# Kernel optimization log

Measured on AMD Instinct MI355X. Metric: run time of the kernel, lower is better.

Reference implementation:

```python
import jax, jax.numpy as jnp
import numpy as np

LPOS, LDIR, H = 10, 4, 256
N = 262144


def posenc(x, L):
    freqs = (2.0 ** jnp.arange(L)).astype(x.dtype)  # [L]
    ang = x[:, None, :] * freqs[:, None]            # [N, L, 3]
    sc = jnp.concatenate([jnp.sin(ang), jnp.cos(ang)], axis=-1)  # [N, L, 6]
    return jnp.concatenate([x, sc.reshape(x.shape[0], L * 6)], axis=1)


def _lin(key, fan_in, fan_out):
    k1, k2 = jax.random.split(key)
    bound = 1.0 / np.sqrt(fan_in)
    w = jax.random.uniform(k1, (fan_out, fan_in), jnp.float32, -bound, bound)
    b = jax.random.uniform(k2, (fan_out,), jnp.float32, -bound, bound)
    return w, b


def setup_inputs() -> dict:
    key = jax.random.key(0)
    ks = jax.random.split(key, 16)
    inp = {
        'xyz': jax.random.normal(ks[0], (N, 3), jnp.float32),
        'd': jax.random.normal(ks[1], (N, 3), jnp.float32),
    }
    in1 = LPOS * 6 + 3  # 63
    dims1 = [(in1, H), (H, H), (H, H), (H, H), (H, H)]
    for i, (fi, fo) in enumerate(dims1):
        w, b = _lin(ks[2 + i], fi, fo)
        inp[f'w1_{i}'], inp[f'b1_{i}'] = w, b
    dims2 = [(H + in1, H), (H, H), (H, H), (H, H + 1)]
    for i, (fi, fo) in enumerate(dims2):
        w, b = _lin(ks[7 + i], fi, fo)
        inp[f'w2_{i}'], inp[f'b2_{i}'] = w, b
    w, b = _lin(ks[11], H + LDIR * 6 + 3, H // 2)
    inp['wr0'], inp['br0'] = w, b
    w, b = _lin(ks[12], H // 2, 3)
    inp['wr1'], inp['br1'] = w, b
    return inp


def reference(xyz, d,
              w1_0, b1_0, w1_1, b1_1, w1_2, b1_2, w1_3, b1_3, w1_4, b1_4,
              w2_0, b2_0, w2_1, b2_1, w2_2, b2_2, w2_3, b2_3,
              wr0, br0, wr1, br1):
    relu = jax.nn.relu
    x_emb = posenc(xyz, LPOS)  # [N, 63]
    d_emb = posenc(d, LDIR)    # [N, 27]
    h = x_emb
    for w, b in ((w1_0, b1_0), (w1_1, b1_1), (w1_2, b1_2), (w1_3, b1_3), (w1_4, b1_4)):
        h = relu(h @ w.T + b)
    h = jnp.concatenate([h, x_emb], axis=1)
    for w, b in ((w2_0, b2_0), (w2_1, b2_1), (w2_2, b2_2)):
        h = relu(h @ w.T + b)
    h = h @ w2_3.T + b2_3  # [N, H+1]
    sigma = h[:, -1]
    h = h[:, :-1]
    # rgb head
    g = relu(jnp.concatenate([h, d_emb], axis=1) @ wr0.T + br0)
    c = jax.nn.sigmoid(g @ wr1.T + br1)  # [N, 3]
    return c, relu(sigma)
```

## Files before the change

kernel.cpp:

```cpp
#include <hip/hip_runtime.h>
#include <hip/hip_bf16.h>

#define NPTS 262144
#define ROWS 64
#define FR 512
#define BUF1_OFF 16384
#define XBUF_OFF 32768
#define LDS_BYTES ((16384*2 + 4096)*2)

typedef __attribute__((ext_vector_type(8))) short short8;
typedef __attribute__((ext_vector_type(4))) float f32x4;

__device__ __forceinline__ ushort bfu(float f) {
  union { float f; unsigned u; } x; x.f = f;
  unsigned r = x.u + 0x7fffu + ((x.u >> 16) & 1u);
  return (ushort)(r >> 16);
}
__device__ __forceinline__ unsigned pk2(float a, float b) {
  __hip_bfloat162 h = __float22bfloat162_rn(float2{a, b});
  return *reinterpret_cast<unsigned*>(&h);
}

__global__ void pack_w(const float* __restrict__ w, ushort* __restrict__ dst,
                       int OUT, int KIN, int nct, int nkt) {
  int t = blockIdx.x * 256 + threadIdx.x;
  int total = nct * nkt * 64;
  if (t >= total) return;
  int l  = t & 63;
  int kt = (t >> 6) % nkt;
  int ct = (t >> 6) / nkt;
  int row = ct * 16 + (l & 15);
  int k0  = kt * 32 + (l >> 4) * 8;
  ushort* d = dst + (size_t)t * 8;
  #pragma unroll
  for (int j = 0; j < 8; ++j) {
    int k = k0 + j;
    float v = (row < OUT && k < KIN) ? w[(size_t)row * KIN + k] : 0.f;
    d[j] = bfu(v);
  }
}

__global__ void pack_b(const float* __restrict__ b, float* __restrict__ dst, int OUT, int OUTP) {
  int i = blockIdx.x * 256 + threadIdx.x;
  if (i < OUTP) dst[i] = (i < OUT) ? b[i] : 0.f;
}

template<int NKT, int KSPLIT, int NC, bool RELU>
__device__ __forceinline__ void layerg(
    const ushort* __restrict__ wpk, const float* __restrict__ bias,
    const ushort* a0, const ushort* a1, int rs1,
    ushort* dst, int ctBase, int lane)
{
  const int lr = lane & 15, lk = lane >> 4;
  f32x4 acc[4][NC];
  #pragma unroll
  for (int c = 0; c < NC; ++c) {
    f32x4 b4 = *(const f32x4*)(bias + (ctBase + c) * 16 + lk * 4);
    #pragma unroll
    for (int r = 0; r < 4; ++r) acc[r][c] = b4;
  }
  #pragma unroll
  for (int kt = 0; kt < NKT; ++kt) {
    short8 av[4];
    #pragma unroll
    for (int r = 0; r < 4; ++r) {
      const ushort* src = (kt < KSPLIT)
        ? (a0 + (r * 8 + kt) * FR + lane * 8)
        : (a1 + (r * rs1 + (kt - KSPLIT)) * FR + lane * 8);
      av[r] = *(const short8*)src;
    }
    #pragma unroll
    for (int c = 0; c < NC; ++c) {
      short8 bv = *(const short8*)(wpk + (size_t)(((ctBase + c) * NKT + kt) * 64 + lane) * 8);
      #pragma unroll
      for (int r = 0; r < 4; ++r)
        acc[r][c] = __builtin_amdgcn_mfma_f32_16x16x32_bf16(bv, av[r], acc[r][c], 0, 0, 0);
    }
  }
  #pragma unroll
  for (int c = 0; c < NC; ++c) {
    const int ct = ctBase + c;
    const int Lp = lr + 16 * ((ct & 1) * 2 + (lk >> 1));
    const int kq = ct >> 1;
    #pragma unroll
    for (int r = 0; r < 4; ++r) {
      float v0 = acc[r][c][0], v1 = acc[r][c][1], v2 = acc[r][c][2], v3 = acc[r][c][3];
      if (RELU) {
        v0 = fmaxf(v0, 0.f); v1 = fmaxf(v1, 0.f);
        v2 = fmaxf(v2, 0.f); v3 = fmaxf(v3, 0.f);
      }
      uint2 p; p.x = pk2(v0, v1); p.y = pk2(v2, v3);
      *(uint2*)(dst + (r * 8 + kq) * FR + Lp * 8 + (lk & 1) * 4) = p;
    }
  }
}

extern __shared__ ushort smem[];

__global__ __launch_bounds__(512, 4) void nerf_fused(
    const float* __restrict__ xyz, const float* __restrict__ dvec,
    const ushort* __restrict__ wp, const float* __restrict__ bp,
    float* __restrict__ out)
{
  ushort* buf0 = smem;
  ushort* buf1 = smem + BUF1_OFF;
  ushort* xbuf = smem + XBUF_OFF;
  const int tid  = threadIdx.x;
  const int row0 = blockIdx.x * ROWS;
  const int wave = tid >> 6, lane = tid & 63;
  const int lr = lane & 15, lk = lane >> 4;

  {
    const int r = wave & 3, kt = wave >> 2;
    const float* x = xyz + (size_t)(row0 + r * 16 + lr) * 3;
    float xv[3] = {x[0], x[1], x[2]};
    const int c0 = kt * 32 + lk * 8;
    unsigned u[4];
    #pragma unroll
    for (int q = 0; q < 4; ++q) {
      ushort h2[2];
      #pragma unroll
      for (int hh = 0; hh < 2; ++hh) {
        int c = c0 + q * 2 + hh;
        float v;
        if (c < 3) v = xv[c];
        else if (c < 63) {
          int idx = c - 3, l = idx / 6, t = idx - l * 6;
          float f = (float)(1 << l);
          float xx = xv[t < 3 ? t : t - 3];
          v = (t < 3) ? __sinf(xx * f) : __cosf(xx * f);
        } else v = 0.f;
        h2[hh] = bfu(v);
      }
      u[q] = (unsigned)h2[0] | ((unsigned)h2[1] << 16);
    }
    uint4* dstv = (uint4*)(xbuf + (r * 2 + kt) * FR + lane * 8);
    *dstv = make_uint4(u[0], u[1], u[2], u[3]);
  }
  __syncthreads();
  layerg<2, 0, 2, true >(wp + 0,      bp + 0,    buf0, xbuf, 2, buf0, wave * 2, lane);
  __syncthreads();
  layerg<8, 8, 2, true >(wp + 16384,  bp + 256,  buf0, xbuf, 2, buf1, wave * 2, lane);
  __syncthreads();
  layerg<8, 8, 2, true >(wp + 81920,  bp + 512,  buf1, xbuf, 2, buf0, wave * 2, lane);
  __syncthreads();
  layerg<8, 8, 2, true >(wp + 147456, bp + 768,  buf0, xbuf, 2, buf1, wave * 2, lane);
  __syncthreads();
  layerg<8, 8, 2, true >(wp + 212992, bp + 1024, buf1, xbuf, 2, buf0, wave * 2, lane);
  __syncthreads();
  layerg<10, 8, 2, true>(wp + 278528, bp + 1280, buf0, xbuf, 2, buf1, wave * 2, lane);
  __syncthreads();
  if (wave < 4) {
    const int r = wave;
    const float* d = dvec + (size_t)(row0 + r * 16 + lr) * 3;
    float dv[3] = {d[0], d[1], d[2]};
    const int c0 = lk * 8;
    unsigned u[4];
    #pragma unroll
    for (int q = 0; q < 4; ++q) {
      ushort h2[2];
      #pragma unroll
      for (int hh = 0; hh < 2; ++hh) {
        int c = c0 + q * 2 + hh;
        float v;
        if (c < 3) v = dv[c];
        else if (c < 27) {
          int idx = c - 3, l = idx / 6, t = idx - l * 6;
          float f = (float)(1 << l);
          float xx = dv[t < 3 ? t : t - 3];
          v = (t < 3) ? __sinf(xx * f) : __cosf(xx * f);
        } else v = 0.f;
        h2[hh] = bfu(v);
      }
      u[q] = (unsigned)h2[0] | ((unsigned)h2[1] << 16);
    }
    uint4* dstv = (uint4*)(xbuf + r * FR + lane * 8);
    *dstv = make_uint4(u[0], u[1], u[2], u[3]);
  }
  layerg<8, 8, 2, true >(wp + 360448, bp + 1536, buf1, xbuf, 2, buf0, wave * 2, lane);
  __syncthreads();
  layerg<8, 8, 2, true >(wp + 425984, bp + 1792, buf0, xbuf, 2, buf1, wave * 2, lane);
  __syncthreads();
  layerg<8, 8, 2, false>(wp + 491520, bp + 2048, buf1, xbuf, 2, buf0, wave * 2, lane);
  if (wave == 0) {
    const ushort* w23 = wp + 491520;
    float bb = bp[2048 + 256 + lr];
    f32x4 acc2[4];
    #pragma unroll
    for (int r = 0; r < 4; ++r) acc2[r] = (f32x4){bb, bb, bb, bb};
    #pragma unroll
    for (int kt = 0; kt < 8; ++kt) {
      short8 bv = *(const short8*)(w23 + (size_t)((16 * 8 + kt) * 64 + lane) * 8);
      #pragma unroll
      for (int r = 0; r < 4; ++r) {
        short8 av = *(const short8*)(buf1 + (r * 8 + kt) * FR + lane * 8);
        acc2[r] = __builtin_amdgcn_mfma_f32_16x16x32_bf16(av, bv, acc2[r], 0, 0, 0);
      }
    }
    if (lr == 0) {
      #pragma unroll
      for (int r = 0; r < 4; ++r)
        #pragma unroll
        for (int i = 0; i < 4; ++i)
          out[(size_t)3 * NPTS + row0 + r * 16 + lk * 4 + i] = fmaxf(acc2[r][i], 0.f);
    }
  }
  __syncthreads();
  layerg<9, 8, 1, true>(wp + 561152, bp + 2320, buf0, xbuf, 1, buf1, wave, lane);
  __syncthreads();
  if (wave < 4) {
    const ushort* w = wp + 598016;
    float bb = bp[2448 + lr];
    f32x4 acc = (f32x4){bb, bb, bb, bb};
    #pragma unroll
    for (int kt = 0; kt < 4; ++kt) {
      short8 av = *(const short8*)(buf1 + (wave * 8 + kt) * FR + lane * 8);
      short8 bv = *(const short8*)(w + (size_t)(kt * 64 + lane) * 8);
      acc = __builtin_amdgcn_mfma_f32_16x16x32_bf16(av, bv, acc, 0, 0, 0);
    }
    if (lr < 3) {
      #pragma unroll
      for (int i = 0; i < 4; ++i) {
        int grow = row0 + wave * 16 + lk * 4 + i;
        out[(size_t)grow * 3 + lr] = 1.f / (1.f + __expf(-acc[i]));
      }
    }
  }
}

extern "C" void kernel_launch(void* const* d_in, const int* in_sizes, int n_in,
                              void* d_out, int out_size, void* d_ws, size_t ws_size,
                              hipStream_t stream) {
  const float* xyz  = (const float*)d_in[0];
  const float* dvec = (const float*)d_in[1];
  ushort* wp = (ushort*)d_ws;
  float*  bp = (float*)((char*)d_ws + 1200128);

  struct WSpec { int idx, OUT, KIN, nct, nkt, off; };
  const WSpec wspecs[11] = {
    { 2, 256,  63, 16,  2,      0},
    { 4, 256, 256, 16,  8,  16384},
    { 6, 256, 256, 16,  8,  81920},
    { 8, 256, 256, 16,  8, 147456},
    {10, 256, 256, 16,  8, 212992},
    {12, 256, 319, 16, 10, 278528},
    {14, 256, 256, 16,  8, 360448},
    {16, 256, 256, 16,  8, 425984},
    {18, 257, 256, 17,  8, 491520},
    {20, 128, 283,  8,  9, 561152},
    {22,   3, 128,  1,  4, 598016},
  };
  for (int i = 0; i < 11; ++i) {
    int total = wspecs[i].nct * wspecs[i].nkt * 64;
    pack_w<<<dim3((total + 255) / 256), dim3(256), 0, stream>>>(
      (const float*)d_in[wspecs[i].idx], wp + wspecs[i].off,
      wspecs[i].OUT, wspecs[i].KIN, wspecs[i].nct, wspecs[i].nkt);
  }
  struct BSpec { int idx, OUT, OUTP, off; };
  const BSpec bspecs[11] = {
    { 3, 256, 256,    0}, { 5, 256, 256,  256}, { 7, 256, 256,  512}, { 9, 256, 256,  768},
    {11, 256, 256, 1024}, {13, 256, 256, 1280}, {15, 256, 256, 1536}, {17, 256, 256, 1792},
    {19, 257, 272, 2048}, {21, 128, 128, 2320}, {23,   3,  16, 2448},
  };
  for (int i = 0; i < 11; ++i) {
    pack_b<<<dim3((bspecs[i].OUTP + 255) / 256), dim3(256), 0, stream>>>(
      (const float*)d_in[bspecs[i].idx], bp + bspecs[i].off, bspecs[i].OUT, bspecs[i].OUTP);
  }

  hipFuncSetAttribute(reinterpret_cast<const void*>(nerf_fused),
                      hipFuncAttributeMaxDynamicSharedMemorySize, LDS_BYTES);
  nerf_fused<<<dim3(NPTS / ROWS), dim3(512), LDS_BYTES, stream>>>(xyz, dvec, wp, bp, (float*)d_out);
}
```

Baseline: 338.1 us.

## Switch fused NeRF MLP from 16x16x32 to 32x32x16 bf16 MFMA tiles

Replaces the 16x16x32 MFMA instruction with 32x32x16 across all layers. The packed weight layout, LDS activation layout, positional-encoding writers, bias padding and workspace offsets all change to match 32-row, 16-k fragments. Each wave now owns one 32-column output tile over two 32-row groups instead of two 16-column tiles over four row groups. The larger tiles give more MACs per operand load and fewer LDS and global weight fetches per FLOP. In exchange each wave holds larger accumulators, which raises register pressure.

```diff
diff --git a/kernel.cpp b/kernel.cpp
--- a/kernel.cpp
+++ b/kernel.cpp
@@ -3,13 +3,13 @@
 
 #define NPTS 262144
 #define ROWS 64
-#define FR 512
 #define BUF1_OFF 16384
 #define XBUF_OFF 32768
 #define LDS_BYTES ((16384*2 + 4096)*2)
 
-typedef __attribute__((ext_vector_type(8))) short short8;
-typedef __attribute__((ext_vector_type(4))) float f32x4;
+typedef __attribute__((ext_vector_type(8)))  short short8;
+typedef __attribute__((ext_vector_type(4)))  float f32x4;
+typedef __attribute__((ext_vector_type(16))) float f32x16;
 
 __device__ __forceinline__ ushort bfu(float f) {
   union { float f; unsigned u; } x; x.f = f;
@@ -29,8 +29,8 @@
   int l  = t & 63;
   int kt = (t >> 6) % nkt;
   int ct = (t >> 6) / nkt;
-  int row = ct * 16 + (l & 15);
-  int k0  = kt * 32 + (l >> 4) * 8;
+  int row = ct * 32 + (l & 31);
+  int k0  = kt * 16 + (l >> 5) * 8;
   ushort* d = dst + (size_t)t * 8;
   #pragma unroll
   for (int j = 0; j < 8; ++j) {
@@ -45,54 +45,67 @@
   if (i < OUTP) dst[i] = (i < OUT) ? b[i] : 0.f;
 }
 
-template<int NKT, int KSPLIT, int NC, bool RELU>
+template<int NKT, int KSPLIT, int NR, bool RELU>
 __device__ __forceinline__ void layerg(
     const ushort* __restrict__ wpk, const float* __restrict__ bias,
-    const ushort* a0, const ushort* a1, int rs1,
-    ushort* dst, int ctBase, int lane)
+    const ushort* a0, int s0, const ushort* a1, int s1,
+    ushort* dst, int ct, int r2base, int lane)
 {
-  const int lr = lane & 15, lk = lane >> 4;
-  f32x4 acc[4][NC];
-  #pragma unroll
-  for (int c = 0; c < NC; ++c) {
-    f32x4 b4 = *(const f32x4*)(bias + (ctBase + c) * 16 + lk * 4);
-    #pragma unroll
-    for (int r = 0; r < 4; ++r) acc[r][c] = b4;
-  }
+  const int l5 = lane >> 5;
+  f32x4 bq[4];
+  #pragma unroll
+  for (int qq = 0; qq < 4; ++qq)
+    bq[qq] = *(const f32x4*)(bias + ct * 32 + qq * 8 + 4 * l5);
+  f32x16 acc[NR];
+  #pragma unroll
+  for (int rr = 0; rr < NR; ++rr)
+    #pragma unroll
+    for (int qq = 0; qq < 4; ++qq) {
+      acc[rr][qq * 4 + 0] = bq[qq][0];
+      acc[rr][qq * 4 + 1] = bq[qq][1];
+      acc[rr][qq * 4 + 2] = bq[qq][2];
+      acc[rr][qq * 4 + 3] = bq[qq][3];
+    }
   #pragma unroll
   for (int kt = 0; kt < NKT; ++kt) {
-    short8 av[4];
-    #pragma unroll
-    for (int r = 0; r < 4; ++r) {
+    short8 bv = *(const short8*)(wpk + (size_t)((ct * NKT + kt) * 64 + lane) * 8);
+    #pragma unroll
+    for (int rr = 0; rr < NR; ++rr) {
+      const int r2 = r2base + rr;
       const ushort* src = (kt < KSPLIT)
-        ? (a0 + (r * 8 + kt) * FR + lane * 8)
-        : (a1 + (r * rs1 + (kt - KSPLIT)) * FR + lane * 8);
-      av[r] = *(const short8*)src;
-    }
-    #pragma unroll
-    for (int c = 0; c < NC; ++c) {
-      short8 bv = *(const short8*)(wpk + (size_t)(((ctBase + c) * NKT + kt) * 64 + lane) * 8);
-      #pragma unroll
-      for (int r = 0; r < 4; ++r)
-        acc[r][c] = __builtin_amdgcn_mfma_f32_16x16x32_bf16(bv, av[r], acc[r][c], 0, 0, 0);
-    }
-  }
-  #pragma unroll
-  for (int c = 0; c < NC; ++c) {
-    const int ct = ctBase + c;
-    const int Lp = lr + 16 * ((ct & 1) * 2 + (lk >> 1));
-    const int kq = ct >> 1;
-    #pragma unroll
-    for (int r = 0; r < 4; ++r) {
-      float v0 = acc[r][c][0], v1 = acc[r][c][1], v2 = acc[r][c][2], v3 = acc[r][c][3];
+          ? a0 + (r2 * s0 + kt) * 512 + lane * 8
+          : a1 + (r2 * s1 + (kt - KSPLIT)) * 512 + lane * 8;
+      short8 av = *(const short8*)src;
+      acc[rr] = __builtin_amdgcn_mfma_f32_32x32x16_bf16(bv, av, acc[rr], 0, 0, 0);
+    }
+  }
+  #pragma unroll
+  for (int rr = 0; rr < NR; ++rr) {
+    const int r2 = r2base + rr;
+    #pragma unroll
+    for (int qq = 0; qq < 4; ++qq) {
+      float v0 = acc[rr][qq * 4 + 0], v1 = acc[rr][qq * 4 + 1];
+      float v2 = acc[rr][qq * 4 + 2], v3 = acc[rr][qq * 4 + 3];
       if (RELU) {
         v0 = fmaxf(v0, 0.f); v1 = fmaxf(v1, 0.f);
         v2 = fmaxf(v2, 0.f); v3 = fmaxf(v3, 0.f);
       }
       uint2 p; p.x = pk2(v0, v1); p.y = pk2(v2, v3);
-      *(uint2*)(dst + (r * 8 + kq) * FR + Lp * 8 + (lk & 1) * 4) = p;
-    }
-  }
+      *(uint2*)(dst + (r2 * 16 + ct * 2 + (qq >> 1)) * 512
+                    + ((lane & 31) + 32 * (qq & 1)) * 8 + 4 * l5) = p;
+    }
+  }
+}
+
+__device__ __forceinline__ float pe_val(const float xv[3], int c, int CMAX) {
+  if (c < 3) return xv[c];
+  if (c < CMAX) {
+    int idx = c - 3, l = idx / 6, t = idx - l * 6;
+    float f = (float)(1 << l);
+    float xx = xv[t < 3 ? t : t - 3];
+    return (t < 3) ? __sinf(xx * f) : __cosf(xx * f);
+  }
+  return 0.f;
 }
 
 extern __shared__ ushort smem[];
@@ -108,122 +121,93 @@
   const int tid  = threadIdx.x;
   const int row0 = blockIdx.x * ROWS;
   const int wave = tid >> 6, lane = tid & 63;
-  const int lr = lane & 15, lk = lane >> 4;
+  const int l5 = lane >> 5;
 
   {
-    const int r = wave & 3, kt = wave >> 2;
-    const float* x = xyz + (size_t)(row0 + r * 16 + lr) * 3;
+    const int r2 = wave >> 2, kt = wave & 3;
+    const float* x = xyz + (size_t)(row0 + r2 * 32 + (lane & 31)) * 3;
     float xv[3] = {x[0], x[1], x[2]};
-    const int c0 = kt * 32 + lk * 8;
+    const int c0 = kt * 16 + l5 * 8;
     unsigned u[4];
     #pragma unroll
-    for (int q = 0; q < 4; ++q) {
-      ushort h2[2];
-      #pragma unroll
-      for (int hh = 0; hh < 2; ++hh) {
-        int c = c0 + q * 2 + hh;
-        float v;
-        if (c < 3) v = xv[c];
-        else if (c < 63) {
-          int idx = c - 3, l = idx / 6, t = idx - l * 6;
-          float f = (float)(1 << l);
-          float xx = xv[t < 3 ? t : t - 3];
-          v = (t < 3) ? __sinf(xx * f) : __cosf(xx * f);
-        } else v = 0.f;
-        h2[hh] = bfu(v);
-      }
-      u[q] = (unsigned)h2[0] | ((unsigned)h2[1] << 16);
-    }
-    uint4* dstv = (uint4*)(xbuf + (r * 2 + kt) * FR + lane * 8);
-    *dstv = make_uint4(u[0], u[1], u[2], u[3]);
-  }
-  __syncthreads();
-  layerg<2, 0, 2, true >(wp + 0,      bp + 0,    buf0, xbuf, 2, buf0, wave * 2, lane);
-  __syncthreads();
-  layerg<8, 8, 2, true >(wp + 16384,  bp + 256,  buf0, xbuf, 2, buf1, wave * 2, lane);
-  __syncthreads();
-  layerg<8, 8, 2, true >(wp + 81920,  bp + 512,  buf1, xbuf, 2, buf0, wave * 2, lane);
-  __syncthreads();
-  layerg<8, 8, 2, true >(wp + 147456, bp + 768,  buf0, xbuf, 2, buf1, wave * 2, lane);
-  __syncthreads();
-  layerg<8, 8, 2, true >(wp + 212992, bp + 1024, buf1, xbuf, 2, buf0, wave * 2, lane);
-  __syncthreads();
-  layerg<10, 8, 2, true>(wp + 278528, bp + 1280, buf0, xbuf, 2, buf1, wave * 2, lane);
+    for (int q = 0; q < 4; ++q)
+      u[q] = (unsigned)bfu(pe_val(xv, c0 + q * 2, 63))
+           | ((unsigned)bfu(pe_val(xv, c0 + q * 2 + 1, 63)) << 16);
+    *(uint4*)(xbuf + (r2 * 4 + kt) * 512 + lane * 8) = make_uint4(u[0], u[1], u[2], u[3]);
+  }
+  __syncthreads();
+  layerg<4, 0, 2, true >(wp + 0,      bp + 0,    xbuf, 4, xbuf, 4, buf0, wave, 0, lane);
+  __syncthreads();
+  layerg<16, 16, 2, true>(wp + 16384,  bp + 256,  buf0, 16, buf0, 16, buf1, wave, 0, lane);
+  __syncthreads();
+  layerg<16, 16, 2, true>(wp + 81920,  bp + 512,  buf1, 16, buf1, 16, buf0, wave, 0, lane);
+  __syncthreads();
+  layerg<16, 16, 2, true>(wp + 147456, bp + 768,  buf0, 16, buf0, 16, buf1, wave, 0, lane);
+  __syncthreads();
+  layerg<16, 16, 2, true>(wp + 212992, bp + 1024, buf1, 16, buf1, 16, buf0, wave, 0, lane);
+  __syncthreads();
+  layerg<20, 16, 2, true>(wp + 278528, bp + 1280, buf0, 16, xbuf, 4, buf1, wave, 0, lane);
   __syncthreads();
   if (wave < 4) {
-    const int r = wave;
-    const float* d = dvec + (size_t)(row0 + r * 16 + lr) * 3;
+    const int r2 = wave >> 1, kt = wave & 1;
+    const float* d = dvec + (size_t)(row0 + r2 * 32 + (lane & 31)) * 3;
     float dv[3] = {d[0], d[1], d[2]};
-    const int c0 = lk * 8;
+    const int c0 = kt * 16 + l5 * 8;
     unsigned u[4];
     #pragma unroll
-    for (int q = 0; q < 4; ++q) {
-      ushort h2[2];
-      #pragma unroll
-      for (int hh = 0; hh < 2; ++hh) {
-        int c = c0 + q * 2 + hh;
-        float v;
-        if (c < 3) v = dv[c];
-        else if (c < 27) {
-          int idx = c - 3, l = idx / 6, t = idx - l * 6;
-          float f = (float)(1 << l);
-          float xx = dv[t < 3 ? t : t - 3];
-          v = (t < 3) ? __sinf(xx * f) : __cosf(xx * f);
-        } else v = 0.f;
-        h2[hh] = bfu(v);
-      }
-      u[q] = (unsigned)h2[0] | ((unsigned)h2[1] << 16);
-    }
-    uint4* dstv = (uint4*)(xbuf + r * FR + lane * 8);
-    *dstv = make_uint4(u[0], u[1], u[2], u[3]);
-  }
-  layerg<8, 8, 2, true >(wp + 360448, bp + 1536, buf1, xbuf, 2, buf0, wave * 2, lane);
-  __syncthreads();
-  layerg<8, 8, 2, true >(wp + 425984, bp + 1792, buf0, xbuf, 2, buf1, wave * 2, lane);
-  __syncthreads();
-  layerg<8, 8, 2, false>(wp + 491520, bp + 2048, buf1, xbuf, 2, buf0, wave * 2, lane);
-  if (wave == 0) {
+    for (int q = 0; q < 4; ++q)
+      u[q] = (unsigned)bfu(pe_val(dv, c0 + q * 2, 27))
+           | ((unsigned)bfu(pe_val(dv, c0 + q * 2 + 1, 27)) << 16);
+    *(uint4*)(xbuf + (r2 * 2 + kt) * 512 + lane * 8) = make_uint4(u[0], u[1], u[2], u[3]);
+  }
+  layerg<16, 16, 2, true>(wp + 360448, bp + 1536, buf1, 16, buf1, 16, buf0, wave, 0, lane);
+  __syncthreads();
+  layerg<16, 16, 2, true>(wp + 425984, bp + 1792, buf0, 16, buf0, 16, buf1, wave, 0, lane);
+  __syncthreads();
+  layerg<16, 16, 2, false>(wp + 491520, bp + 2048, buf1, 16, buf1, 16, buf0, wave, 0, lane);
+  if (wave < 2) {
     const ushort* w23 = wp + 491520;
-    float bb = bp[2048 + 256 + lr];
-    f32x4 acc2[4];
-    #pragma unroll
-    for (int r = 0; r < 4; ++r) acc2[r] = (f32x4){bb, bb, bb, bb};
+    const int r2 = wave;
+    f32x16 acc;
+    #pragma unroll
+    for (int qq = 0; qq < 4; ++qq) {
+      f32x4 b4 = *(const f32x4*)(bp + 2048 + 256 + qq * 8 + 4 * l5);
+      acc[qq * 4 + 0] = b4[0]; acc[qq * 4 + 1] = b4[1];
+      acc[qq * 4 + 2] = b4[2]; acc[qq * 4 + 3] = b4[3];
+    }
+    #pragma unroll
+    for (int kt = 0; kt < 16; ++kt) {
+      short8 bv = *(const short8*)(w23 + (size_t)((8 * 16 + kt) * 64 + lane) * 8);
+      short8 av = *(const short8*)(buf1 + (r2 * 16 + kt) * 512 + lane * 8);
+      acc = __builtin_amdgcn_mfma_f32_32x32x16_bf16(bv, av, acc, 0, 0, 0);
+    }
+    if (lane < 32)
+      out[(size_t)3 * NPTS + row0 + r2 * 32 + lane] = fmaxf(acc[0], 0.f);
+  }
+  __syncthreads();
+  layerg<18, 16, 1, true>(wp + 565248, bp + 2336, buf0, 16, xbuf, 2, buf1, wave & 3, wave >> 2, lane);
+  __syncthreads();
+  if (wave < 2) {
+    const ushort* w = wp + 602112;
+    const int r2 = wave;
+    f32x16 acc;
+    #pragma unroll
+    for (int qq = 0; qq < 4; ++qq) {
+      f32x4 b4 = *(const f32x4*)(bp + 2464 + qq * 8 + 4 * l5);
+      acc[qq * 4 + 0] = b4[0]; acc[qq * 4 + 1] = b4[1];
+      acc[qq * 4 + 2] = b4[2]; acc[qq * 4 + 3] = b4[3];
+    }
     #pragma unroll
     for (int kt = 0; kt < 8; ++kt) {
-      short8 bv = *(const short8*)(w23 + (size_t)((16 * 8 + kt) * 64 + lane) * 8);
-      #pragma unroll
-      for (int r = 0; r < 4; ++r) {
-        short8 av = *(const short8*)(buf1 + (r * 8 + kt) * FR + lane * 8);
-        acc2[r] = __builtin_amdgcn_mfma_f32_16x16x32_bf16(av, bv, acc2[r], 0, 0, 0);
-      }
-    }
-    if (lr == 0) {
-      #pragma unroll
-      for (int r = 0; r < 4; ++r)
-        #pragma unroll
-        for (int i = 0; i < 4; ++i)
-          out[(size_t)3 * NPTS + row0 + r * 16 + lk * 4 + i] = fmaxf(acc2[r][i], 0.f);
-    }
-  }
-  __syncthreads();
-  layerg<9, 8, 1, true>(wp + 561152, bp + 2320, buf0, xbuf, 1, buf1, wave, lane);
-  __syncthreads();
-  if (wave < 4) {
-    const ushort* w = wp + 598016;
-    float bb = bp[2448 + lr];
-    f32x4 acc = (f32x4){bb, bb, bb, bb};
-    #pragma unroll
-    for (int kt = 0; kt < 4; ++kt) {
-      short8 av = *(const short8*)(buf1 + (wave * 8 + kt) * FR + lane * 8);
       short8 bv = *(const short8*)(w + (size_t)(kt * 64 + lane) * 8);
-      acc = __builtin_amdgcn_mfma_f32_16x16x32_bf16(av, bv, acc, 0, 0, 0);
-    }
-    if (lr < 3) {
-      #pragma unroll
-      for (int i = 0; i < 4; ++i) {
-        int grow = row0 + wave * 16 + lk * 4 + i;
-        out[(size_t)grow * 3 + lr] = 1.f / (1.f + __expf(-acc[i]));
-      }
+      short8 av = *(const short8*)(buf1 + (r2 * 16 + kt) * 512 + lane * 8);
+      acc = __builtin_amdgcn_mfma_f32_32x32x16_bf16(bv, av, acc, 0, 0, 0);
+    }
+    if (lane < 32) {
+      int p = row0 + r2 * 32 + lane;
+      out[(size_t)p * 3 + 0] = 1.f / (1.f + __expf(-acc[0]));
+      out[(size_t)p * 3 + 1] = 1.f / (1.f + __expf(-acc[1]));
+      out[(size_t)p * 3 + 2] = 1.f / (1.f + __expf(-acc[2]));
     }
   }
 }
@@ -234,21 +218,21 @@
   const float* xyz  = (const float*)d_in[0];
   const float* dvec = (const float*)d_in[1];
   ushort* wp = (ushort*)d_ws;
-  float*  bp = (float*)((char*)d_ws + 1200128);
+  float*  bp = (float*)((char*)d_ws + 1212416);
 
   struct WSpec { int idx, OUT, KIN, nct, nkt, off; };
   const WSpec wspecs[11] = {
-    { 2, 256,  63, 16,  2,      0},
-    { 4, 256, 256, 16,  8,  16384},
-    { 6, 256, 256, 16,  8,  81920},
-    { 8, 256, 256, 16,  8, 147456},
-    {10, 256, 256, 16,  8, 212992},
-    {12, 256, 319, 16, 10, 278528},
-    {14, 256, 256, 16,  8, 360448},
-    {16, 256, 256, 16,  8, 425984},
-    {18, 257, 256, 17,  8, 491520},
-    {20, 128, 283,  8,  9, 561152},
-    {22,   3, 128,  1,  4, 598016},
+    { 2, 256,  63, 8,  4,      0},
+    { 4, 256, 256, 8, 16,  16384},
+    { 6, 256, 256, 8, 16,  81920},
+    { 8, 256, 256, 8, 16, 147456},
+    {10, 256, 256, 8, 16, 212992},
+    {12, 256, 319, 8, 20, 278528},
+    {14, 256, 256, 8, 16, 360448},
+    {16, 256, 256, 8, 16, 425984},
+    {18, 257, 256, 9, 16, 491520},
+    {20, 128, 283, 4, 18, 565248},
+    {22,   3, 128, 1,  8, 602112},
   };
   for (int i = 0; i < 11; ++i) {
     int total = wspecs[i].nct * wspecs[i].nkt * 64;
@@ -260,7 +244,7 @@
   const BSpec bspecs[11] = {
     { 3, 256, 256,    0}, { 5, 256, 256,  256}, { 7, 256, 256,  512}, { 9, 256, 256,  768},
     {11, 256, 256, 1024}, {13, 256, 256, 1280}, {15, 256, 256, 1536}, {17, 256, 256, 1792},
-    {19, 257, 272, 2048}, {21, 128, 128, 2320}, {23,   3,  16, 2448},
+    {19, 257, 288, 2048}, {21, 128, 128, 2336}, {23,   3,  32, 2464},
   };
   for (int i = 0; i < 11; ++i) {
     pack_b<<<dim3((bspecs[i].OUTP + 255) / 256), dim3(256), 0, stream>>>(
```

After: 380.3 us. 1.12x slower.

## Retile per-wave MLP work to 2 row tiles by 4 column tiles

Applied to the files above, without the earlier changes.

Each wave previously computed all 4 row tiles for 2 column tiles, so every wave reread the full activation tile from LDS and only 2 weight fragments per k-step. Now the 8 waves form a 4x2 grid: each covers 2 row tiles by 4 column tiles (2x2 for the rgb layer). The goal is to halve LDS activation reads per wave and spread weight-load reuse differently. Each wave now loads twice as many global weight fragments, and the accumulator register count is unchanged.

```diff
diff --git a/kernel.cpp b/kernel.cpp
--- a/kernel.cpp
+++ b/kernel.cpp
@@ -45,35 +45,35 @@
   if (i < OUTP) dst[i] = (i < OUT) ? b[i] : 0.f;
 }
 
-template<int NKT, int KSPLIT, int NC, bool RELU>
+template<int NKT, int KSPLIT, int NC, int NR, bool RELU>
 __device__ __forceinline__ void layerg(
     const ushort* __restrict__ wpk, const float* __restrict__ bias,
-    const ushort* a0, const ushort* a1, int rs1,
-    ushort* dst, int ctBase, int lane)
+    const ushort* a0, int s0, const ushort* a1, int s1,
+    ushort* dst, int ctBase, int rBase, int lane)
 {
   const int lr = lane & 15, lk = lane >> 4;
-  f32x4 acc[4][NC];
+  f32x4 acc[NR][NC];
   #pragma unroll
   for (int c = 0; c < NC; ++c) {
     f32x4 b4 = *(const f32x4*)(bias + (ctBase + c) * 16 + lk * 4);
     #pragma unroll
-    for (int r = 0; r < 4; ++r) acc[r][c] = b4;
+    for (int r = 0; r < NR; ++r) acc[r][c] = b4;
   }
   #pragma unroll
   for (int kt = 0; kt < NKT; ++kt) {
-    short8 av[4];
-    #pragma unroll
-    for (int r = 0; r < 4; ++r) {
-      const ushort* src = (kt < KSPLIT)
-        ? (a0 + (r * 8 + kt) * FR + lane * 8)
-        : (a1 + (r * rs1 + (kt - KSPLIT)) * FR + lane * 8);
-      av[r] = *(const short8*)src;
+    short8 av[NR];
+    #pragma unroll
+    for (int r = 0; r < NR; ++r) {
+      const int rt = rBase + r;
+      av[r] = (kt < KSPLIT)
+        ? *(const short8*)(a0 + (size_t)(rt * s0 + kt) * FR + lane * 8)
+        : *(const short8*)(a1 + (size_t)(rt * s1 + (kt - KSPLIT)) * FR + lane * 8);
     }
     #pragma unroll
     for (int c = 0; c < NC; ++c) {
       short8 bv = *(const short8*)(wpk + (size_t)(((ctBase + c) * NKT + kt) * 64 + lane) * 8);
       #pragma unroll
-      for (int r = 0; r < 4; ++r)
+      for (int r = 0; r < NR; ++r)
         acc[r][c] = __builtin_amdgcn_mfma_f32_16x16x32_bf16(bv, av[r], acc[r][c], 0, 0, 0);
     }
   }
@@ -83,14 +83,15 @@
     const int Lp = lr + 16 * ((ct & 1) * 2 + (lk >> 1));
     const int kq = ct >> 1;
     #pragma unroll
-    for (int r = 0; r < 4; ++r) {
+    for (int r = 0; r < NR; ++r) {
+      const int rt = rBase + r;
       float v0 = acc[r][c][0], v1 = acc[r][c][1], v2 = acc[r][c][2], v3 = acc[r][c][3];
       if (RELU) {
         v0 = fmaxf(v0, 0.f); v1 = fmaxf(v1, 0.f);
         v2 = fmaxf(v2, 0.f); v3 = fmaxf(v3, 0.f);
       }
       uint2 p; p.x = pk2(v0, v1); p.y = pk2(v2, v3);
-      *(uint2*)(dst + (r * 8 + kq) * FR + Lp * 8 + (lk & 1) * 4) = p;
+      *(uint2*)(dst + (size_t)(rt * 8 + kq) * FR + Lp * 8 + (lk & 1) * 4) = p;
     }
   }
 }
@@ -109,6 +110,7 @@
   const int row0 = blockIdx.x * ROWS;
   const int wave = tid >> 6, lane = tid & 63;
   const int lr = lane & 15, lk = lane >> 4;
+  const int cg = wave & 3, rg = wave >> 2;
 
   {
     const int r = wave & 3, kt = wave >> 2;
@@ -134,21 +136,20 @@
       }
       u[q] = (unsigned)h2[0] | ((unsigned)h2[1] << 16);
     }
-    uint4* dstv = (uint4*)(xbuf + (r * 2 + kt) * FR + lane * 8);
-    *dstv = make_uint4(u[0], u[1], u[2], u[3]);
-  }
-  __syncthreads();
-  layerg<2, 0, 2, true >(wp + 0,      bp + 0,    buf0, xbuf, 2, buf0, wave * 2, lane);
-  __syncthreads();
-  layerg<8, 8, 2, true >(wp + 16384,  bp + 256,  buf0, xbuf, 2, buf1, wave * 2, lane);
-  __syncthreads();
-  layerg<8, 8, 2, true >(wp + 81920,  bp + 512,  buf1, xbuf, 2, buf0, wave * 2, lane);
-  __syncthreads();
-  layerg<8, 8, 2, true >(wp + 147456, bp + 768,  buf0, xbuf, 2, buf1, wave * 2, lane);
-  __syncthreads();
-  layerg<8, 8, 2, true >(wp + 212992, bp + 1024, buf1, xbuf, 2, buf0, wave * 2, lane);
-  __syncthreads();
-  layerg<10, 8, 2, true>(wp + 278528, bp + 1280, buf0, xbuf, 2, buf1, wave * 2, lane);
+    *(uint4*)(xbuf + (size_t)(r * 2 + kt) * FR + lane * 8) = make_uint4(u[0], u[1], u[2], u[3]);
+  }
+  __syncthreads();
+  layerg<2, 0, 4, 2, true >(wp + 0,      bp + 0,    xbuf, 2, xbuf, 2, buf0, cg * 4, rg * 2, lane);
+  __syncthreads();
+  layerg<8, 8, 4, 2, true >(wp + 16384,  bp + 256,  buf0, 8, buf0, 8, buf1, cg * 4, rg * 2, lane);
+  __syncthreads();
+  layerg<8, 8, 4, 2, true >(wp + 81920,  bp + 512,  buf1, 8, buf1, 8, buf0, cg * 4, rg * 2, lane);
+  __syncthreads();
+  layerg<8, 8, 4, 2, true >(wp + 147456, bp + 768,  buf0, 8, buf0, 8, buf1, cg * 4, rg * 2, lane);
+  __syncthreads();
+  layerg<8, 8, 4, 2, true >(wp + 212992, bp + 1024, buf1, 8, buf1, 8, buf0, cg * 4, rg * 2, lane);
+  __syncthreads();
+  layerg<10, 8, 4, 2, true>(wp + 278528, bp + 1280, buf0, 8, xbuf, 2, buf1, cg * 4, rg * 2, lane);
   __syncthreads();
   if (wave < 4) {
     const int r = wave;
@@ -174,14 +175,13 @@
       }
       u[q] = (unsigned)h2[0] | ((unsigned)h2[1] << 16);
     }
-    uint4* dstv = (uint4*)(xbuf + r * FR + lane * 8);
-    *dstv = make_uint4(u[0], u[1], u[2], u[3]);
-  }
-  layerg<8, 8, 2, true >(wp + 360448, bp + 1536, buf1, xbuf, 2, buf0, wave * 2, lane);
-  __syncthreads();
-  layerg<8, 8, 2, true >(wp + 425984, bp + 1792, buf0, xbuf, 2, buf1, wave * 2, lane);
-  __syncthreads();
-  layerg<8, 8, 2, false>(wp + 491520, bp + 2048, buf1, xbuf, 2, buf0, wave * 2, lane);
+    *(uint4*)(xbuf + (size_t)r * FR + lane * 8) = make_uint4(u[0], u[1], u[2], u[3]);
+  }
+  layerg<8, 8, 4, 2, true >(wp + 360448, bp + 1536, buf1, 8, buf1, 8, buf0, cg * 4, rg * 2, lane);
+  __syncthreads();
+  layerg<8, 8, 4, 2, true >(wp + 425984, bp + 1792, buf0, 8, buf0, 8, buf1, cg * 4, rg * 2, lane);
+  __syncthreads();
+  layerg<8, 8, 4, 2, false>(wp + 491520, bp + 2048, buf1, 8, buf1, 8, buf0, cg * 4, rg * 2, lane);
   if (wave == 0) {
     const ushort* w23 = wp + 491520;
     float bb = bp[2048 + 256 + lr];
@@ -193,7 +193,7 @@
       short8 bv = *(const short8*)(w23 + (size_t)((16 * 8 + kt) * 64 + lane) * 8);
       #pragma unroll
       for (int r = 0; r < 4; ++r) {
-        short8 av = *(const short8*)(buf1 + (r * 8 + kt) * FR + lane * 8);
+        short8 av = *(const short8*)(buf1 + (size_t)(r * 8 + kt) * FR + lane * 8);
         acc2[r] = __builtin_amdgcn_mfma_f32_16x16x32_bf16(av, bv, acc2[r], 0, 0, 0);
       }
     }
@@ -206,7 +206,7 @@
     }
   }
   __syncthreads();
-  layerg<9, 8, 1, true>(wp + 561152, bp + 2320, buf0, xbuf, 1, buf1, wave, lane);
+  layerg<9, 8, 2, 2, true>(wp + 561152, bp + 2320, buf0, 8, xbuf, 1, buf1, cg * 2, rg * 2, lane);
   __syncthreads();
   if (wave < 4) {
     const ushort* w = wp + 598016;
@@ -214,7 +214,7 @@
     f32x4 acc = (f32x4){bb, bb, bb, bb};
     #pragma unroll
     for (int kt = 0; kt < 4; ++kt) {
-      short8 av = *(const short8*)(buf1 + (wave * 8 + kt) * FR + lane * 8);
+      short8 av = *(const short8*)(buf1 + (size_t)(wave * 8 + kt) * FR + lane * 8);
       short8 bv = *(const short8*)(w + (size_t)(kt * 64 + lane) * 8);
       acc = __builtin_amdgcn_mfma_f32_16x16x32_bf16(av, bv, acc, 0, 0, 0);
     }
```

Result: slower. 590.6 us (+74.7%).
